# Optimization experiments

Measured on AMD Instinct MI355X. Metric: run time of the kernel, lower is better.

Reference implementation:

```python
import jax, jax.numpy as jnp
import numpy as np

FEAT_DIM = 16
NUM_DEPTHS = 64


def _lookat(p):
    z = p / np.linalg.norm(p)
    up = np.array([0.0, 1.0, 0.0])
    x = np.cross(up, z); x = x / np.linalg.norm(x)
    y = np.cross(z, x)
    m = np.eye(4)
    m[:3, 0] = x; m[:3, 1] = y; m[:3, 2] = z; m[:3, 3] = p
    return m


def setup_inputs() -> dict:
    key = jax.random.key(0)
    ks = jax.random.split(key, 6)
    S, Vin, Vt, C, D, H, W = 2, 3, 4, FEAT_DIM, NUM_DEPTHS, 96, 96
    enc = jax.random.normal(ks[0], (S, Vin, C, D, H, W), jnp.float32) * 0.5
    rng = np.random.default_rng(0)

    def poses(n):
        ps = rng.normal(size=(S, n, 3))
        ps = ps / np.linalg.norm(ps, axis=-1, keepdims=True) * 1.3
        return jnp.asarray(np.stack([[_lookat(ps[i, j]) for j in range(n)] for i in range(S)]), jnp.float32)

    input_poses = poses(Vin)
    target_poses = poses(Vt)
    W1 = jax.random.normal(ks[1], (16, 64), jnp.float32) * 0.25
    W2 = jax.random.normal(ks[2], (64, 64), jnp.float32) * 0.125
    W3 = jax.random.normal(ks[3], (64, 17), jnp.float32) * 0.125
    return dict(
        encoded_imgs=enc, input_poses=input_poses, target_poses=target_poses,
        focal=1.2, z_near=0.8, z_far=1.8, samples_per_ray=64,
        W1=W1, b1=jnp.zeros((64,), jnp.float32),
        W2=W2, b2=jnp.zeros((64,), jnp.float32),
        W3=W3, b3=jnp.zeros((17,), jnp.float32),
    )


def grid_sample_3d(vol, grid):
    # vol: (N,C,D,H,W); grid: (N,P,3) xyz in [-1,1]; trilinear, zero padding, align_corners=False
    N, C, D, H, W = vol.shape
    P = grid.shape[1]
    ix = ((grid[..., 0] + 1.0) * W - 1.0) * 0.5
    iy = ((grid[..., 1] + 1.0) * H - 1.0) * 0.5
    iz = ((grid[..., 2] + 1.0) * D - 1.0) * 0.5
    x0, y0, z0 = jnp.floor(ix), jnp.floor(iy), jnp.floor(iz)
    volf = vol.reshape(N, C, D * H * W)
    out = jnp.zeros((N, C, P), vol.dtype)
    for dz in (0, 1):
        for dy in (0, 1):
            for dx in (0, 1):
                xc, yc, zc = x0 + dx, y0 + dy, z0 + dz
                wgt = (1.0 - jnp.abs(ix - xc)) * (1.0 - jnp.abs(iy - yc)) * (1.0 - jnp.abs(iz - zc))
                valid = ((xc >= 0) & (xc < W) & (yc >= 0) & (yc < H) & (zc >= 0) & (zc < D))
                xi = jnp.clip(xc, 0, W - 1).astype(jnp.int32)
                yi = jnp.clip(yc, 0, H - 1).astype(jnp.int32)
                zi = jnp.clip(zc, 0, D - 1).astype(jnp.int32)
                idx = (zi * H + yi) * W + xi  # (N,P)
                vals = jnp.take_along_axis(volf, idx[:, None, :], axis=2)  # (N,C,P)
                out = out + (wgt * valid)[:, None, :] * vals
    return out


def _upsample2_align_corners(x):
    # bilinear x2 on last two axes, align_corners=True (torch UpsamplingBilinear2d)
    def interp(x, axis):
        n = x.shape[axis]
        m = 2 * n
        pos = jnp.arange(m) * ((n - 1) / (m - 1))
        lo = jnp.floor(pos).astype(jnp.int32)
        hi = jnp.minimum(lo + 1, n - 1)
        f = (pos - lo).astype(x.dtype)
        xl = jnp.take(x, lo, axis=axis)
        xh = jnp.take(x, hi, axis=axis)
        shp = [1] * x.ndim; shp[axis] = m
        f = f.reshape(shp)
        return xl * (1.0 - f) + xh * f
    return interp(interp(x, -2), -1)


def _forward(encoded_imgs, input_poses, target_poses, focal, z_near, z_far,
             samples_per_ray, W1, b1, W2, b2, W3, b3):
    S, Vin, C, D, H, W = encoded_imgs.shape
    Vt = target_poses.shape[1]
    h, w = H // 2, W // 2
    spr = samples_per_ray
    dt = encoded_imgs.dtype

    # --- gen_rays at half resolution ---
    poses = target_poses.reshape(S * Vt, 4, 4)
    ys = ((jnp.arange(h, dtype=dt) + 0.5) / h) * 2.0 - 1.0
    xs = ((jnp.arange(w, dtype=dt) + 0.5) / w) * 2.0 - 1.0
    yy, xx = jnp.meshgrid(ys, xs, indexing='ij')
    dirs_cam = jnp.stack([xx / focal, -yy / focal, -jnp.ones_like(xx)], -1)  # (h,w,3)
    dirs = jnp.einsum('bij,hwj->bhwi', poses[:, :3, :3], dirs_cam)            # (B,h,w,3)
    origins = poses[:, None, None, :3, 3]                                      # (B,1,1,3)

    t = z_near + (z_far - z_near) * (jnp.arange(spr, dtype=dt) / (spr - 1))
    times = jnp.broadcast_to(t, (S * Vt, h, w, spr))
    pts = origins[..., None, :] + times[..., None] * dirs[..., None, :]        # (B,h,w,spr,3)

    times = times.reshape(S, Vt, h, w, spr)
    pts = pts.reshape(S, Vt, h, w, spr, 3)
    pts_h = jnp.concatenate([pts, jnp.ones_like(pts[..., :1])], axis=-1)      # (S,Vt,h,w,spr,4)

    # --- invert input poses (rigid) ---
    R = input_poses[..., :3, :3]
    tr = input_poses[..., :3, 3]
    Rt = jnp.swapaxes(R, -1, -2)
    inv_t = -jnp.einsum('svij,svj->svi', Rt, tr)
    top = jnp.concatenate([Rt, inv_t[..., None]], axis=-1)                     # (S,Vin,3,4)
    bottom = jnp.broadcast_to(jnp.array([0.0, 0.0, 0.0, 1.0], dt), (S, Vin, 1, 4))
    extrinsics = jnp.concatenate([top, bottom], axis=-2)                       # (S,Vin,4,4)

    local = jnp.einsum('svij,sthwpj->svthwpi', extrinsics, pts_h)              # (S,Vin,Vt,h,w,spr,4)
    x = local[..., 0]
    y = local[..., 1]
    z = -local[..., 2]
    u = x / z * focal
    v = y / z * focal
    min_z, max_z = focal * z_near, focal * z_far
    wd = 2.0 * (z - min_z) / (max_z - min_z) - 1.0
    uvw = jnp.stack((u, -v, -wd), axis=-1)                                     # (S,Vin,Vt,h,w,spr,3)

    feats = grid_sample_3d(encoded_imgs.reshape(S * Vin, C, D, H, W),
                           uvw.reshape(S * Vin, -1, 3))                        # (S*Vin,C,P)
    feats = feats.reshape(S, Vin, C, Vt, h, w, spr)
    feats = jnp.mean(feats, axis=1)                                            # baseline_mean camera weighting
    feats = jnp.transpose(feats, (0, 2, 3, 4, 5, 1))                           # (S,Vt,h,w,spr,C)

    # --- MLP with residual feature skip ---
    x1 = jax.nn.relu(feats @ W1 + b1)
    x2 = jax.nn.relu(x1 @ W2 + b2)
    out = x2 @ W3 + b3                                                         # (...,17)
    density = jax.nn.relu(out[..., 0])
    rgb = feats + out[..., 1:]

    # --- volume rendering ---
    deltas = times[..., 1:] - times[..., :-1]
    last = jnp.full_like(deltas[..., :1], 1e10)
    deltas = jnp.concatenate([deltas, last], axis=-1)
    sigdel = density * deltas
    alpha = 1.0 - jnp.exp(-sigdel)
    transmittance = jnp.exp(-jnp.cumsum(sigdel, axis=-1))
    wts = alpha * transmittance
    renders = jnp.sum(wts[..., None] * rgb, axis=-2)                           # (S,Vt,h,w,16)

    renders = jnp.transpose(renders, (0, 1, 4, 2, 3))                          # (S,Vt,16,h,w)
    renders = _upsample2_align_corners(renders.reshape(S * Vt, C, h, w))
    return renders.reshape(S, Vt, C, H, W)


def reference(encoded_imgs, input_poses, target_poses, focal, z_near, z_far,
              samples_per_ray, W1, b1, W2, b2, W3, b3):
    return _forward(encoded_imgs, input_poses, target_poses, float(focal), float(z_near),
                    float(z_far), int(samples_per_ray), W1, b1, W2, b2, W3, b3)
```

## Files before the change

### kernel.cpp

```cpp
#include <hip/hip_runtime.h>
#include <hip/hip_bf16.h>
#include <math.h>

#define NS   2
#define NVIN 3
#define NVT  4
#define NC   16
#define ND   64
#define NH   96
#define NW   96
#define HWH  48
#define SPR  64
#define DHW  (ND*NH*NW)
#define NTILE (DHW / 64)
#define NSAMP (NS*NVT*HWH*HWH*SPR)
#define NRAYS (NS*NVT*HWH*HWH)

typedef __attribute__((ext_vector_type(8))) short bfrag;
typedef __attribute__((ext_vector_type(4))) float cfrag;

#define MFMA16 __builtin_amdgcn_mfma_f32_16x16x32_bf16

#define WAVE_LDS_SYNC() asm volatile("s_waitcnt lgkmcnt(0)" ::: "memory")

__device__ __forceinline__ short f2bf(float x) {
    union { __hip_bfloat16 b; short s; } cv;
    cv.b = __float2bfloat16(x);
    return cv.s;
}
__device__ __forceinline__ float bf2f(short s) {
    union { unsigned int u; float f; } cv;
    cv.u = ((unsigned int)(unsigned short)s) << 16;
    return cv.f;
}

__device__ __forceinline__ void mk_frag(const float* p, bfrag& ah, bfrag& al) {
    float4 v0 = *(const float4*)p;
    float4 v1 = *(const float4*)(p + 4);
    float e[8] = {v0.x, v0.y, v0.z, v0.w, v1.x, v1.y, v1.z, v1.w};
    #pragma unroll
    for (int j = 0; j < 8; j++) {
        short h = f2bf(e[j]);
        ah[j] = h;
        al[j] = f2bf(e[j] - bf2f(h));
    }
}

__global__ __launch_bounds__(256) void wprep_kernel(
    const float* __restrict__ W1, const float* __restrict__ W2,
    const float* __restrict__ W3, short* __restrict__ whi, short* __restrict__ wlo)
{
    int t = blockIdx.x * 256 + threadIdx.x;
    int f = t >> 6, L = t & 63;
    int q = L >> 4, li = L & 15;
    #pragma unroll
    for (int j = 0; j < 8; j++) {
        int kloc = q * 8 + j;
        float w = 0.f;
        if (f < 4) {
            int n = f * 16 + li, k = kloc;
            if (k < 16) w = W1[k * 64 + n];
        } else if (f < 12) {
            int kt = (f - 4) >> 2, nt = (f - 4) & 3;
            w = W2[(kt * 32 + kloc) * 64 + nt * 16 + li];
        } else {
            int kt = (f - 12) >> 1, nt = (f - 12) & 1;
            int n = nt * 16 + li;
            if (n < 17) w = W3[(kt * 32 + kloc) * 17 + n];
        }
        short h = f2bf(w);
        whi[(f * 64 + L) * 8 + j] = h;
        wlo[(f * 64 + L) * 8 + j] = f2bf(w - bf2f(h));
    }
}

__global__ __launch_bounds__(256) void transpose_kernel(
    const float* __restrict__ in, float* __restrict__ out)
{
    __shared__ float tile[NC][64 + 4];
    const int t   = threadIdx.x;
    const int blk = blockIdx.x;
    const int vox0 = (blk % NTILE) * 64;
    const int sv   = blk / NTILE;

    const int c  = t >> 4;
    const int vg = (t & 15) * 4;
    const float* src = in + ((size_t)sv * NC + c) * DHW + vox0 + vg;
    float4 v = *(const float4*)src;
    tile[c][vg + 0] = v.x; tile[c][vg + 1] = v.y;
    tile[c][vg + 2] = v.z; tile[c][vg + 3] = v.w;
    __syncthreads();

    const int ov = t >> 2;
    const int oc = (t & 3) * 4;
    float4 w = make_float4(tile[oc + 0][ov], tile[oc + 1][ov],
                           tile[oc + 2][ov], tile[oc + 3][ov]);
    float* dst = out + ((size_t)sv * DHW + vox0 + ov) * NC + oc;
    *(float4*)dst = w;
}

__global__ __launch_bounds__(256) void gather_kernel(
    const float* __restrict__ enc_t,
    const float* __restrict__ ipose,
    const float* __restrict__ tpose,
    const float* __restrict__ focal_p,
    const float* __restrict__ znear_p,
    const float* __restrict__ zfar_p,
    float* __restrict__ xbuf)
{
    const int ray  = (blockIdx.x & 7) * (NRAYS >> 3) + (blockIdx.x >> 3);
    const int lane = threadIdx.x & 63;
    const int wv   = threadIdx.x >> 6;
    const int c4   = lane & 3;
    const int xbit = (lane >> 2) & 1;
    const int ds   = lane >> 3;
    const int px   = ray % HWH;
    const int py   = (ray / HWH) % HWH;
    const int b    = ray / (HWH * HWH);
    const int s    = b >> 2;

    const float focal = focal_p[0];
    const float znear = znear_p[0];
    const float zfar  = zfar_p[0];

    const float* P = tpose + b * 16;
    float ysc = ((py + 0.5f) / (float)HWH) * 2.f - 1.f;
    float xsc = ((px + 0.5f) / (float)HWH) * 2.f - 1.f;
    float dcx = xsc / focal, dcy = -ysc / focal, dcz = -1.f;
    float dirx = P[0]*dcx + P[1]*dcy + P[2]*dcz;
    float diry = P[4]*dcx + P[5]*dcy + P[6]*dcz;
    float dirz = P[8]*dcx + P[9]*dcy + P[10]*dcz;

    float lox[NVIN], loy[NVIN], loz[NVIN];
    float ldx[NVIN], ldy[NVIN], ldz[NVIN];
    #pragma unroll
    for (int v = 0; v < NVIN; v++) {
        const float* E = ipose + (s * NVIN + v) * 16;
        float qx = P[3] - E[3], qy = P[7] - E[7], qz = P[11] - E[11];
        lox[v] = E[0]*qx + E[4]*qy + E[8]*qz;
        loy[v] = E[1]*qx + E[5]*qy + E[9]*qz;
        loz[v] = E[2]*qx + E[6]*qy + E[10]*qz;
        ldx[v] = E[0]*dirx + E[4]*diry + E[8]*dirz;
        ldy[v] = E[1]*dirx + E[5]*diry + E[9]*dirz;
        ldz[v] = E[2]*dirx + E[6]*diry + E[10]*dirz;
    }

    const float minz = focal * znear, maxz = focal * zfar;
    const float inv3 = 1.f / 3.f;

    #pragma unroll 1
    for (int iter = 0; iter < 2; iter++) {
        const int d = wv * 8 + ds + iter * 32;
        float tv = znear + (zfar - znear) * ((float)d / (float)(SPR - 1));

        float wgt[12];
        int   off[12];
        #pragma unroll
        for (int v = 0; v < NVIN; v++) {
            float lx = lox[v] + tv * ldx[v];
            float ly = loy[v] + tv * ldy[v];
            float lz = loz[v] + tv * ldz[v];
            float zz = -lz;
            float u  = lx / zz * focal;
            float vv = ly / zz * focal;
            float wd = 2.f * (zz - minz) / (maxz - minz) - 1.f;
            float ix = ((u   + 1.f) * NW - 1.f) * 0.5f;
            float iy = ((-vv + 1.f) * NH - 1.f) * 0.5f;
            float iz = ((-wd + 1.f) * ND - 1.f) * 0.5f;
            float x0 = floorf(ix), y0 = floorf(iy), z0 = floorf(iz);
            float x1 = x0 + 1.f,   y1 = y0 + 1.f,   z1 = z0 + 1.f;

            float wxa0 = 1.f - fabsf(ix - x0), wxa1 = 1.f - fabsf(ix - x1);
            float wya0 = 1.f - fabsf(iy - y0), wya1 = 1.f - fabsf(iy - y1);
            float wza0 = 1.f - fabsf(iz - z0), wza1 = 1.f - fabsf(iz - z1);
            wxa0 = (x0 >= 0.f && x0 < (float)NW) ? wxa0 : 0.f;
            wxa1 = (x1 >= 0.f && x1 < (float)NW) ? wxa1 : 0.f;
            wya0 = (y0 >= 0.f && y0 < (float)NH) ? wya0 : 0.f;
            wya1 = (y1 >= 0.f && y1 < (float)NH) ? wya1 : 0.f;
            wza0 = (z0 >= 0.f && z0 < (float)ND) ? wza0 : 0.f;
            wza1 = (z1 >= 0.f && z1 < (float)ND) ? wza1 : 0.f;

            int xi0 = min(max((int)x0, 0), NW - 1), xi1 = min(max((int)x1, 0), NW - 1);
            int yi0 = min(max((int)y0, 0), NH - 1), yi1 = min(max((int)y1, 0), NH - 1);
            int zi0 = min(max((int)z0, 0), ND - 1), zi1 = min(max((int)z1, 0), ND - 1);
            int o00 = (zi0 * NH + yi0) * NW, o01 = (zi0 * NH + yi1) * NW;
            int o10 = (zi1 * NH + yi0) * NW, o11 = (zi1 * NH + yi1) * NW;

            float wxl = xbit ? wxa1 : wxa0;
            int   xil = xbit ? xi1  : xi0;

            wgt[v*4 + 0] = (wxl * wya0) * wza0;  off[v*4 + 0] = (o00 + xil) * NC + c4 * 4;
            wgt[v*4 + 1] = (wxl * wya1) * wza0;  off[v*4 + 1] = (o01 + xil) * NC + c4 * 4;
            wgt[v*4 + 2] = (wxl * wya0) * wza1;  off[v*4 + 2] = (o10 + xil) * NC + c4 * 4;
            wgt[v*4 + 3] = (wxl * wya1) * wza1;  off[v*4 + 3] = (o11 + xil) * NC + c4 * 4;
        }

        float4 av[12];
        #pragma unroll
        for (int j = 0; j < 12; j++) {
            const float* VB = enc_t + (size_t)(s * NVIN + (j >> 2)) * DHW * NC;
            av[j] = *(const float4*)(VB + off[j]);
        }

        float f0 = 0.f, f1 = 0.f, f2 = 0.f, f3 = 0.f;
        #pragma unroll
        for (int j = 0; j < 12; j++) {
            f0 += wgt[j] * av[j].x; f1 += wgt[j] * av[j].y;
            f2 += wgt[j] * av[j].z; f3 += wgt[j] * av[j].w;
        }
        f0 += __shfl_xor(f0, 4, 64);
        f1 += __shfl_xor(f1, 4, 64);
        f2 += __shfl_xor(f2, 4, 64);
        f3 += __shfl_xor(f3, 4, 64);

        if (!xbit)
            ((float4*)xbuf)[(ray * 64 + d) * 4 + c4] =
                make_float4(f0 * inv3, f1 * inv3, f2 * inv3, f3 * inv3);
    }
}

__global__ __launch_bounds__(256) void mlp_kernel(
    const float* __restrict__ xbuf,
    const float* __restrict__ znear_p,
    const float* __restrict__ zfar_p,
    const short* __restrict__ whi, const short* __restrict__ wlo,
    const float* __restrict__ B1, const float* __restrict__ B2,
    const float* __restrict__ B3,
    float* __restrict__ rhalf)
{
    const int lane = threadIdx.x & 63;
    const int ray  = blockIdx.x * 4 + (threadIdx.x >> 6);
    const int px   = ray % HWH;
    const int py   = (ray / HWH) % HWH;
    const int b    = ray / (HWH * HWH);

    const float znear = znear_p[0];
    const float zfar  = zfar_p[0];

    __shared__ float sbuf[4][64][36];
    float (*B)[36] = sbuf[threadIdx.x >> 6];
    const int li = lane & 15, q = lane >> 4;
    const float* X = xbuf + (size_t)ray * 64 * NC;

    float b1v[4], b2v[4], b3v[2];
    #pragma unroll
    for (int nt = 0; nt < 4; nt++) { b1v[nt] = B1[nt*16 + li]; b2v[nt] = B2[nt*16 + li]; }
    b3v[0] = B3[li];
    b3v[1] = (li == 0) ? B3[16] : 0.f;

    bfrag xah[4], xal[4];
    bfrag zb = {0,0,0,0,0,0,0,0};
    #pragma unroll
    for (int mt = 0; mt < 4; mt++) {
        if (q < 2) mk_frag(X + (mt*16 + li) * NC + q * 8, xah[mt], xal[mt]);
        else { xah[mt] = zb; xal[mt] = zb; }
    }

    cfrag zc = {0.f, 0.f, 0.f, 0.f};
    cfrag h2acc[4][4];
    #pragma unroll
    for (int mt = 0; mt < 4; mt++)
        #pragma unroll
        for (int nt = 0; nt < 4; nt++) h2acc[mt][nt] = zc;

    #pragma unroll
    for (int c1 = 0; c1 < 2; c1++) {
        cfrag h1[4][2];
        #pragma unroll
        for (int nt2 = 0; nt2 < 2; nt2++) {
            int f = 2*c1 + nt2;
            bfrag bh = *(const bfrag*)(whi + (f*64 + lane)*8);
            bfrag bl = *(const bfrag*)(wlo + (f*64 + lane)*8);
            #pragma unroll
            for (int mt = 0; mt < 4; mt++) {
                cfrag a = zc;
                a = MFMA16(xal[mt], bh, a, 0, 0, 0);
                a = MFMA16(xah[mt], bl, a, 0, 0, 0);
                a = MFMA16(xah[mt], bh, a, 0, 0, 0);
                h1[mt][nt2] = a;
            }
        }
        WAVE_LDS_SYNC();
        #pragma unroll
        for (int mt = 0; mt < 4; mt++)
            #pragma unroll
            for (int nt2 = 0; nt2 < 2; nt2++)
                #pragma unroll
                for (int r = 0; r < 4; r++)
                    B[mt*16 + q*4 + r][nt2*16 + li] =
                        fmaxf(h1[mt][nt2][r] + b1v[2*c1 + nt2], 0.f);
        WAVE_LDS_SYNC();
        bfrag hah[4], hal[4];
        #pragma unroll
        for (int mt = 0; mt < 4; mt++)
            mk_frag(&B[mt*16 + li][q*8], hah[mt], hal[mt]);
        #pragma unroll
        for (int nt = 0; nt < 4; nt++) {
            int f = 4 + c1*4 + nt;
            bfrag bh = *(const bfrag*)(whi + (f*64 + lane)*8);
            bfrag bl = *(const bfrag*)(wlo + (f*64 + lane)*8);
            #pragma unroll
            for (int mt = 0; mt < 4; mt++) {
                cfrag a = h2acc[mt][nt];
                a = MFMA16(hal[mt], bh, a, 0, 0, 0);
                a = MFMA16(hah[mt], bl, a, 0, 0, 0);
                a = MFMA16(hah[mt], bh, a, 0, 0, 0);
                h2acc[mt][nt] = a;
            }
        }
    }

    cfrag oacc[4][2];
    #pragma unroll
    for (int mt = 0; mt < 4; mt++)
        #pragma unroll
        for (int nt = 0; nt < 2; nt++) oacc[mt][nt] = zc;

    #pragma unroll
    for (int c2 = 0; c2 < 2; c2++) {
        WAVE_LDS_SYNC();
        #pragma unroll
        for (int mt = 0; mt < 4; mt++)
            #pragma unroll
            for (int nt2 = 0; nt2 < 2; nt2++)
                #pragma unroll
                for (int r = 0; r < 4; r++)
                    B[mt*16 + q*4 + r][nt2*16 + li] =
                        fmaxf(h2acc[mt][2*c2 + nt2][r] + b2v[2*c2 + nt2], 0.f);
        WAVE_LDS_SYNC();
        bfrag hah[4], hal[4];
        #pragma unroll
        for (int mt = 0; mt < 4; mt++)
            mk_frag(&B[mt*16 + li][q*8], hah[mt], hal[mt]);
        #pragma unroll
        for (int nt = 0; nt < 2; nt++) {
            int f = 12 + c2*2 + nt;
            bfrag bh = *(const bfrag*)(whi + (f*64 + lane)*8);
            bfrag bl = *(const bfrag*)(wlo + (f*64 + lane)*8);
            #pragma unroll
            for (int mt = 0; mt < 4; mt++) {
                cfrag a = oacc[mt][nt];
                a = MFMA16(hal[mt], bh, a, 0, 0, 0);
                a = MFMA16(hah[mt], bl, a, 0, 0, 0);
                a = MFMA16(hah[mt], bh, a, 0, 0, 0);
                oacc[mt][nt] = a;
            }
        }
    }

    WAVE_LDS_SYNC();
    #pragma unroll
    for (int mt = 0; mt < 4; mt++)
        #pragma unroll
        for (int nt = 0; nt < 2; nt++) {
            int ch = nt*16 + li;
            if (ch < 17) {
                #pragma unroll
                for (int r = 0; r < 4; r++)
                    B[mt*16 + q*4 + r][ch] = oacc[mt][nt][r] + b3v[nt];
            }
        }
    WAVE_LDS_SYNC();
    float4 o0 = *(float4*)&B[lane][0];
    float4 o1 = *(float4*)&B[lane][4];
    float4 o2 = *(float4*)&B[lane][8];
    float4 o3 = *(float4*)&B[lane][12];
    float o16 = B[lane][16];

    float density = fmaxf(o0.x, 0.f);
    float orgb[16] = {o0.y, o0.z, o0.w, o1.x, o1.y, o1.z, o1.w, o2.x,
                      o2.y, o2.z, o2.w, o3.x, o3.y, o3.z, o3.w, o16};

    float4 fx0 = *(const float4*)(X + lane * NC + 0);
    float4 fx1 = *(const float4*)(X + lane * NC + 4);
    float4 fx2 = *(const float4*)(X + lane * NC + 8);
    float4 fx3 = *(const float4*)(X + lane * NC + 12);
    float feats[16] = {fx0.x, fx0.y, fx0.z, fx0.w, fx1.x, fx1.y, fx1.z, fx1.w,
                       fx2.x, fx2.y, fx2.z, fx2.w, fx3.x, fx3.y, fx3.z, fx3.w};

    float tv = znear + (zfar - znear) * ((float)lane / (float)(SPR - 1));
    float tn = znear + (zfar - znear) * ((float)(lane + 1) / (float)(SPR - 1));
    float delta = (lane < SPR - 1) ? (tn - tv) : 1e10f;
    float sigdel = density * delta;
    float alpha = 1.f - expf(-sigdel);
    float csum = sigdel;
    #pragma unroll
    for (int off = 1; off < 64; off <<= 1) {
        float nb = __shfl_up(csum, off, 64);
        if (lane >= off) csum += nb;
    }
    float wray = alpha * expf(-csum);

    #pragma unroll
    for (int c = 0; c < NC; c++) {
        float val = wray * (feats[c] + orgb[c]);
        #pragma unroll
        for (int off = 32; off >= 1; off >>= 1)
            val += __shfl_down(val, off, 64);
        if (lane == 0)
            rhalf[((b * NC + c) * HWH + py) * HWH + px] = val;
    }
}

__device__ __forceinline__ void mlp_and_composite(
    const float feats[NC], int lane, int b, int py, int px,
    float tv, float znear, float zfar,
    const float* __restrict__ W1, const float* __restrict__ B1,
    const float* __restrict__ W2, const float* __restrict__ B2,
    const float* __restrict__ W3, const float* __restrict__ B3,
    float* __restrict__ rhalf)
{
    float outa[17];
    #pragma unroll
    for (int c = 0; c < 17; c++) outa[c] = B3[c];
    for (int kc = 0; kc < 4; kc++) {
        float h2c[16];
        #pragma unroll
        for (int k = 0; k < 16; k++) h2c[k] = B2[kc * 16 + k];
        #pragma unroll 4
        for (int j = 0; j < 64; j++) {
            float a = B1[j];
            #pragma unroll
            for (int i = 0; i < NC; i++) a += feats[i] * W1[i * 64 + j];
            a = fmaxf(a, 0.f);
            const float* w2p = W2 + j * 64 + kc * 16;
            #pragma unroll
            for (int k = 0; k < 16; k++) h2c[k] += a * w2p[k];
        }
        #pragma unroll
        for (int k = 0; k < 16; k++) {
            float hv = fmaxf(h2c[k], 0.f);
            const float* w3p = W3 + (kc * 16 + k) * 17;
            #pragma unroll
            for (int c = 0; c < 17; c++) outa[c] += hv * w3p[c];
        }
    }
    float density = fmaxf(outa[0], 0.f);
    float tn = znear + (zfar - znear) * ((float)(lane + 1) / (float)(SPR - 1));
    float delta = (lane < SPR - 1) ? (tn - tv) : 1e10f;
    float sigdel = density * delta;
    float alpha = 1.f - expf(-sigdel);
    float csum = sigdel;
    #pragma unroll
    for (int off = 1; off < 64; off <<= 1) {
        float nb = __shfl_up(csum, off, 64);
        if (lane >= off) csum += nb;
    }
    float wray = alpha * expf(-csum);
    #pragma unroll
    for (int c = 0; c < NC; c++) {
        float val = wray * (feats[c] + outa[1 + c]);
        #pragma unroll
        for (int off = 32; off >= 1; off >>= 1)
            val += __shfl_down(val, off, 64);
        if (lane == 0)
            rhalf[((b * NC + c) * HWH + py) * HWH + px] = val;
    }
}

__global__ __launch_bounds__(256) void render_kernel(
    const float* __restrict__ enc,
    const float* __restrict__ ipose,
    const float* __restrict__ tpose,
    const float* __restrict__ focal_p,
    const float* __restrict__ znear_p,
    const float* __restrict__ zfar_p,
    const float* __restrict__ W1, const float* __restrict__ B1,
    const float* __restrict__ W2, const float* __restrict__ B2,
    const float* __restrict__ W3, const float* __restrict__ B3,
    float* __restrict__ rhalf)
{
    const int lane = threadIdx.x & 63;
    const int ray  = blockIdx.x * 4 + (threadIdx.x >> 6);
    const int px   = ray % HWH;
    const int py   = (ray / HWH) % HWH;
    const int b    = ray / (HWH * HWH);
    const int s    = b >> 2;
    const float focal = focal_p[0];
    const float znear = znear_p[0];
    const float zfar  = zfar_p[0];
    const float* P = tpose + b * 16;
    float ysc = ((py + 0.5f) / (float)HWH) * 2.f - 1.f;
    float xsc = ((px + 0.5f) / (float)HWH) * 2.f - 1.f;
    float dcx = xsc / focal, dcy = -ysc / focal, dcz = -1.f;
    float dirx = P[0]*dcx + P[1]*dcy + P[2]*dcz;
    float diry = P[4]*dcx + P[5]*dcy + P[6]*dcz;
    float dirz = P[8]*dcx + P[9]*dcy + P[10]*dcz;
    float tv  = znear + (zfar - znear) * ((float)lane / (float)(SPR - 1));
    float ptx = P[3] + tv * dirx, pty = P[7] + tv * diry, ptz = P[11] + tv * dirz;
    float feats[NC];
    #pragma unroll
    for (int c = 0; c < NC; c++) feats[c] = 0.f;
    const float minz = focal * znear, maxz = focal * zfar;
    for (int v = 0; v < NVIN; v++) {
        const float* E = ipose + (s * NVIN + v) * 16;
        float qx = ptx - E[3], qy = pty - E[7], qz = ptz - E[11];
        float lx = E[0]*qx + E[4]*qy + E[8]*qz;
        float ly = E[1]*qx + E[5]*qy + E[9]*qz;
        float lz = E[2]*qx + E[6]*qy + E[10]*qz;
        float zz = -lz;
        float u  = lx / zz * focal;
        float vv = ly / zz * focal;
        float wd = 2.f * (zz - minz) / (maxz - minz) - 1.f;
        float ix = ((u   + 1.f) * NW - 1.f) * 0.5f;
        float iy = ((-vv + 1.f) * NH - 1.f) * 0.5f;
        float iz = ((-wd + 1.f) * ND - 1.f) * 0.5f;
        float x0 = floorf(ix), y0 = floorf(iy), z0 = floorf(iz);
        float wgt[8]; int idx[8];
        #pragma unroll
        for (int k = 0; k < 8; k++) {
            float xc = x0 + (k & 1), yc = y0 + ((k >> 1) & 1), zc = z0 + (k >> 2);
            float wt = (1.f - fabsf(ix - xc)) * (1.f - fabsf(iy - yc)) * (1.f - fabsf(iz - zc));
            bool valid = (xc >= 0.f) && (xc < (float)NW) &&
                         (yc >= 0.f) && (yc < (float)NH) &&
                         (zc >= 0.f) && (zc < (float)ND);
            wgt[k] = valid ? wt : 0.f;
            int xi = min(max((int)xc, 0), NW - 1);
            int yi = min(max((int)yc, 0), NH - 1);
            int zi = min(max((int)zc, 0), ND - 1);
            idx[k] = (zi * NH + yi) * NW + xi;
        }
        const float* VB = enc + (size_t)(s * NVIN + v) * NC * DHW;
        #pragma unroll
        for (int c = 0; c < NC; c++) {
            const float* vc = VB + c * DHW;
            float acc = 0.f;
            #pragma unroll
            for (int k = 0; k < 8; k++) acc += wgt[k] * vc[idx[k]];
            feats[c] += acc;
        }
    }
    #pragma unroll
    for (int c = 0; c < NC; c++) feats[c] *= (1.f / 3.f);
    mlp_and_composite(feats, lane, b, py, px, tv, znear, zfar,
                      W1, B1, W2, B2, W3, B3, rhalf);
}

__global__ __launch_bounds__(256) void upsample_kernel(
    const float* __restrict__ in, float* __restrict__ out)
{
    int tid = blockIdx.x * 256 + threadIdx.x;
    int ox = tid % NW;
    int oy = (tid / NW) % NH;
    int c  = (tid / (NW * NH)) % NC;
    int b  = tid / (NW * NH * NC);
    const float sc = (float)((HWH - 1) / (double)(NH - 1));
    float pyf = oy * sc;
    float pxf = ox * sc;
    int y0 = (int)floorf(pyf); int y1 = min(y0 + 1, HWH - 1); float fy = pyf - y0;
    int x0 = (int)floorf(pxf); int x1 = min(x0 + 1, HWH - 1); float fx = pxf - x0;
    const float* src = in + (b * NC + c) * HWH * HWH;
    float v00 = src[y0 * HWH + x0], v01 = src[y0 * HWH + x1];
    float v10 = src[y1 * HWH + x0], v11 = src[y1 * HWH + x1];
    float gl = v00 * (1.f - fy) + v10 * fy;
    float gr = v01 * (1.f - fy) + v11 * fy;
    out[tid] = gl * (1.f - fx) + gr * fx;
}

extern "C" void kernel_launch(void* const* d_in, const int* in_sizes, int n_in,
                              void* d_out, int out_size, void* d_ws, size_t ws_size,
                              hipStream_t stream) {
    const float* enc   = (const float*)d_in[0];
    const float* ipose = (const float*)d_in[1];
    const float* tpose = (const float*)d_in[2];
    const float* focal = (const float*)d_in[3];
    const float* znear = (const float*)d_in[4];
    const float* zfar  = (const float*)d_in[5];
    const float* W1 = (const float*)d_in[7];
    const float* B1 = (const float*)d_in[8];
    const float* W2 = (const float*)d_in[9];
    const float* B2 = (const float*)d_in[10];
    const float* W3 = (const float*)d_in[11];
    const float* B3 = (const float*)d_in[12];

    float* out = (float*)d_out;
    const int nrays = NRAYS;
    const int nout  = NS * NVT * NC * NH * NW;
    const size_t enc_t_bytes = (size_t)NS * NVIN * NC * DHW * 4;
    const size_t rhalf_bytes = (size_t)nrays * NC * 4;
    const size_t wfrag_bytes = 16 * 64 * 8 * sizeof(short);
    const size_t xbuf_bytes  = (size_t)NSAMP * NC * 4;

    if (ws_size >= enc_t_bytes + rhalf_bytes + 2 * wfrag_bytes + xbuf_bytes) {
        char* base = (char*)d_ws;
        float* enc_t = (float*)base;                      base += enc_t_bytes;
        float* rhalf = (float*)base;                      base += rhalf_bytes;
        short* whi   = (short*)base;                      base += wfrag_bytes;
        short* wlo   = (short*)base;                      base += wfrag_bytes;
        float* xbuf  = (float*)base;

        wprep_kernel<<<4, 256, 0, stream>>>(W1, W2, W3, whi, wlo);
        transpose_kernel<<<NS * NVIN * NTILE, 256, 0, stream>>>(enc, enc_t);
        gather_kernel<<<nrays, 256, 0, stream>>>(
            enc_t, ipose, tpose, focal, znear, zfar, xbuf);
        mlp_kernel<<<nrays / 4, 256, 0, stream>>>(
            xbuf, znear, zfar, whi, wlo, B1, B2, B3, rhalf);
        upsample_kernel<<<nout / 256, 256, 0, stream>>>(rhalf, out);
    } else {
        float* rhalf = (float*)d_ws;
        render_kernel<<<nrays / 4, 256, 0, stream>>>(
            enc, ipose, tpose, focal, znear, zfar,
            W1, B1, W2, B2, W3, B3, rhalf);
        upsample_kernel<<<nout / 256, 256, 0, stream>>>(rhalf, out);
    }
}
```

Before: 607.4 us.

## Restructure gather: per-sample coordinate math staged in LDS, wave per ray

The gather kernel now assigns one ray per wave and one depth sample per lane to compute projection, trilinear weights and corner offsets once, storing them in shared memory. Four passes then read these records and issue eight explicit global vector loads per view for 16 samples by 4 channel groups, accumulating in registers. This removes redundant per-lane coordinate math and reduces block count, at the cost of about 53KB LDS per block (lower occupancy) and a full memory wait per view that serialises load latency.

```diff
diff --git a/kernel.cpp b/kernel.cpp
--- a/kernel.cpp
+++ b/kernel.cpp
@@ -18,6 +18,8 @@
 
 typedef __attribute__((ext_vector_type(8))) short bfrag;
 typedef __attribute__((ext_vector_type(4))) float cfrag;
+typedef __attribute__((ext_vector_type(4))) float f32x4;
+typedef __attribute__((ext_vector_type(4))) int   i32x4;
 
 #define MFMA16 __builtin_amdgcn_mfma_f32_16x16x32_bf16
 
@@ -108,12 +110,10 @@
     const float* __restrict__ zfar_p,
     float* __restrict__ xbuf)
 {
-    const int ray  = (blockIdx.x & 7) * (NRAYS >> 3) + (blockIdx.x >> 3);
+    const int blk  = (blockIdx.x & 7) * ((NRAYS / 4) >> 3) + (blockIdx.x >> 3);
     const int lane = threadIdx.x & 63;
     const int wv   = threadIdx.x >> 6;
-    const int c4   = lane & 3;
-    const int xbit = (lane >> 2) & 1;
-    const int ds   = lane >> 3;
+    const int ray  = blk * 4 + wv;
     const int px   = ray % HWH;
     const int py   = (ray / HWH) % HWH;
     const int b    = ray / (HWH * HWH);
@@ -122,6 +122,8 @@
     const float focal = focal_p[0];
     const float znear = znear_p[0];
     const float zfar  = zfar_p[0];
+
+    __shared__ float lds[4 * 64 * 52];
 
     const float* P = tpose + b * 16;
     float ysc = ((py + 0.5f) / (float)HWH) * 2.f - 1.f;
@@ -148,13 +150,10 @@
     const float minz = focal * znear, maxz = focal * zfar;
     const float inv3 = 1.f / 3.f;
 
-    #pragma unroll 1
-    for (int iter = 0; iter < 2; iter++) {
-        const int d = wv * 8 + ds + iter * 32;
+    {
+        const int d = lane;
         float tv = znear + (zfar - znear) * ((float)d / (float)(SPR - 1));
-
-        float wgt[12];
-        int   off[12];
+        float* row = lds + (wv * 64 + d) * 52;
         #pragma unroll
         for (int v = 0; v < NVIN; v++) {
             float lx = lox[v] + tv * ldx[v];
@@ -186,36 +185,61 @@
             int o00 = (zi0 * NH + yi0) * NW, o01 = (zi0 * NH + yi1) * NW;
             int o10 = (zi1 * NH + yi0) * NW, o11 = (zi1 * NH + yi1) * NW;
 
-            float wxl = xbit ? wxa1 : wxa0;
-            int   xil = xbit ? xi1  : xi0;
-
-            wgt[v*4 + 0] = (wxl * wya0) * wza0;  off[v*4 + 0] = (o00 + xil) * NC + c4 * 4;
-            wgt[v*4 + 1] = (wxl * wya1) * wza0;  off[v*4 + 1] = (o01 + xil) * NC + c4 * 4;
-            wgt[v*4 + 2] = (wxl * wya0) * wza1;  off[v*4 + 2] = (o10 + xil) * NC + c4 * 4;
-            wgt[v*4 + 3] = (wxl * wya1) * wza1;  off[v*4 + 3] = (o11 + xil) * NC + c4 * 4;
-        }
-
-        float4 av[12];
-        #pragma unroll
-        for (int j = 0; j < 12; j++) {
-            const float* VB = enc_t + (size_t)(s * NVIN + (j >> 2)) * DHW * NC;
-            av[j] = *(const float4*)(VB + off[j]);
-        }
-
-        float f0 = 0.f, f1 = 0.f, f2 = 0.f, f3 = 0.f;
-        #pragma unroll
-        for (int j = 0; j < 12; j++) {
-            f0 += wgt[j] * av[j].x; f1 += wgt[j] * av[j].y;
-            f2 += wgt[j] * av[j].z; f3 += wgt[j] * av[j].w;
-        }
-        f0 += __shfl_xor(f0, 4, 64);
-        f1 += __shfl_xor(f1, 4, 64);
-        f2 += __shfl_xor(f2, 4, 64);
-        f3 += __shfl_xor(f3, 4, 64);
-
-        if (!xbit)
-            ((float4*)xbuf)[(ray * 64 + d) * 4 + c4] =
-                make_float4(f0 * inv3, f1 * inv3, f2 * inv3, f3 * inv3);
+            const int sb = (s * NVIN + v) * (DHW * NC * 4);
+
+            f32x4 w0 = { (wxa0*wya0)*wza0, (wxa1*wya0)*wza0,
+                         (wxa0*wya1)*wza0, (wxa1*wya1)*wza0 };
+            f32x4 w1 = { (wxa0*wya0)*wza1, (wxa1*wya0)*wza1,
+                         (wxa0*wya1)*wza1, (wxa1*wya1)*wza1 };
+            i32x4 o0 = { sb + (o00 + xi0) * 64, sb + (o00 + xi1) * 64,
+                         sb + (o01 + xi0) * 64, sb + (o01 + xi1) * 64 };
+            i32x4 o1 = { sb + (o10 + xi0) * 64, sb + (o10 + xi1) * 64,
+                         sb + (o11 + xi0) * 64, sb + (o11 + xi1) * 64 };
+
+            *(f32x4*)(row + v*16 + 0)  = w0;
+            *(f32x4*)(row + v*16 + 4)  = w1;
+            *(i32x4*)(row + v*16 + 8)  = o0;
+            *(i32x4*)(row + v*16 + 12) = o1;
+        }
+    }
+    WAVE_LDS_SYNC();
+
+    const int c4 = lane & 3;
+    const int cb = c4 * 16;
+
+    #pragma unroll 1
+    for (int pass = 0; pass < 4; pass++) {
+        const int sm = pass * 16 + (lane >> 2);
+        const float* row = lds + (wv * 64 + sm) * 52;
+        f32x4 acc = {0.f, 0.f, 0.f, 0.f};
+
+        #pragma unroll
+        for (int v = 0; v < NVIN; v++) {
+            f32x4 wq0 = *(const f32x4*)(row + v*16 + 0);
+            f32x4 wq1 = *(const f32x4*)(row + v*16 + 4);
+            i32x4 oq0 = *(const i32x4*)(row + v*16 + 8);
+            i32x4 oq1 = *(const i32x4*)(row + v*16 + 12);
+
+            f32x4 a0, a1, a2, a3, a4, a5, a6, a7;
+            int v0 = oq0.x + cb, v1 = oq0.y + cb, v2 = oq0.z + cb, v3 = oq0.w + cb;
+            int v4 = oq1.x + cb, v5 = oq1.y + cb, v6 = oq1.z + cb, v7 = oq1.w + cb;
+            asm volatile("global_load_dwordx4 %0, %1, %2" : "=&v"(a0) : "v"(v0), "s"(enc_t));
+            asm volatile("global_load_dwordx4 %0, %1, %2" : "=&v"(a1) : "v"(v1), "s"(enc_t));
+            asm volatile("global_load_dwordx4 %0, %1, %2" : "=&v"(a2) : "v"(v2), "s"(enc_t));
+            asm volatile("global_load_dwordx4 %0, %1, %2" : "=&v"(a3) : "v"(v3), "s"(enc_t));
+            asm volatile("global_load_dwordx4 %0, %1, %2" : "=&v"(a4) : "v"(v4), "s"(enc_t));
+            asm volatile("global_load_dwordx4 %0, %1, %2" : "=&v"(a5) : "v"(v5), "s"(enc_t));
+            asm volatile("global_load_dwordx4 %0, %1, %2" : "=&v"(a6) : "v"(v6), "s"(enc_t));
+            asm volatile("global_load_dwordx4 %0, %1, %2" : "=&v"(a7) : "v"(v7), "s"(enc_t));
+            asm volatile("s_waitcnt vmcnt(0)" ::: "memory");
+            __builtin_amdgcn_sched_barrier(0);
+
+            acc += wq0.x * a0;  acc += wq0.y * a1;
+            acc += wq0.z * a2;  acc += wq0.w * a3;
+            acc += wq1.x * a4;  acc += wq1.y * a5;
+            acc += wq1.z * a6;  acc += wq1.w * a7;
+        }
+        ((f32x4*)xbuf)[(ray * 64 + sm) * 4 + c4] = acc * inv3;
     }
 }
 
@@ -591,7 +615,7 @@
 
         wprep_kernel<<<4, 256, 0, stream>>>(W1, W2, W3, whi, wlo);
         transpose_kernel<<<NS * NVIN * NTILE, 256, 0, stream>>>(enc, enc_t);
-        gather_kernel<<<nrays, 256, 0, stream>>>(
+        gather_kernel<<<nrays / 4, 256, 0, stream>>>(
             enc_t, ipose, tpose, focal, znear, zfar, xbuf);
         mlp_kernel<<<nrays / 4, 256, 0, stream>>>(
             xbuf, znear, zfar, whi, wlo, B1, B2, B3, rhalf);
```

Result: no change. 598.3 us (-1.5%).
